# Performance work log

Measured on AMD Instinct MI355X. Metric: run time of the kernel, lower is better.

Reference implementation:

```python
import jax, jax.numpy as jnp
import numpy as np

CHEB_K = 3
HIDDEN = 64
HORIZON = 12
OUT_DIM = 1


def _supports(E, K):
    # adaptive adjacency: softmax(relu(E E^T)) rows, Chebyshev polynomial stack [K, N, N]
    A = jax.nn.softmax(jax.nn.relu(E @ E.T), axis=1)
    N = E.shape[0]
    s = [jnp.eye(N, dtype=E.dtype), A]
    for _ in range(2, K):
        s.append(2.0 * (A @ s[-1]) - s[-2])
    return jnp.stack(s, axis=0)


def _gconv(x, supports, W, b):
    # x: [B,N,C], supports: [K,N,N], W: [N,K,C,O], b: [N,O] -> [B,N,O]
    xg = jnp.einsum('knm,bmc->bnkc', supports, x)
    return jnp.einsum('bnkc,nkco->bno', xg, W) + b


def _agcrn_layer(x_seq, supports, gW, gb, uW, ub):
    # x_seq: [B,T,N,C]; returns full hidden sequence [B,T,N,H]
    B, T, N, _ = x_seq.shape
    h0 = jnp.zeros((B, N, HIDDEN), dtype=x_seq.dtype)

    def step(h, x):
        zr = jax.nn.sigmoid(_gconv(jnp.concatenate([x, h], axis=-1), supports, gW, gb))
        z, r = zr[..., :HIDDEN], zr[..., HIDDEN:]
        hc = jnp.tanh(_gconv(jnp.concatenate([x, z * h], axis=-1), supports, uW, ub))
        h_new = r * h + (1.0 - r) * hc
        return h_new, h_new

    _, hs = jax.lax.scan(step, h0, jnp.swapaxes(x_seq, 0, 1))  # [T,B,N,H]
    return jnp.swapaxes(hs, 0, 1)


def _forward(source, E, pools, conv_w, conv_b):
    supports = _supports(E, CHEB_K)
    cur = source
    for (gwp, gbp, uwp, ubp) in pools:
        # per-node weights from embedding pool (hoisted: E is constant over time)
        gW = jnp.einsum('nd,dkio->nkio', E, gwp)
        gb = E @ gbp
        uW = jnp.einsum('nd,dkio->nkio', E, uwp)
        ub = E @ ubp
        cur = _agcrn_layer(cur, supports, gW, gb, uW, ub)
    last = cur[:, -1]  # [B,N,H]
    # end_conv: Conv2d(1, horizon*out_dim, kernel=(1,H)) == linear over H per node
    y = jnp.einsum('bnh,oh->bon', last, conv_w) + conv_b[None, :, None]  # [B, horizon*out, N]
    B, _, N = y.shape
    y = y.reshape(B, HORIZON, OUT_DIM, N).transpose(0, 1, 3, 2)  # [B, horizon, N, out_dim]
    return y


def setup_inputs() -> dict:
    key = jax.random.key(0)
    ks = jax.random.split(key, 12)
    B, T, N, C, D, H = 64, 12, 2000, 1, 16, HIDDEN
    s = 0.1  # keep gates/tanh unsaturated
    return {
        'source': jax.random.normal(ks[0], (B, T, N, C), jnp.float32),
        'node_embeddings': jax.random.normal(ks[1], (N, D), jnp.float32),
        'gate_wpool_0': jax.random.normal(ks[2], (D, CHEB_K, C + H, 2 * H), jnp.float32) * s,
        'gate_bpool_0': jax.random.normal(ks[3], (D, 2 * H), jnp.float32) * s,
        'update_wpool_0': jax.random.normal(ks[4], (D, CHEB_K, C + H, H), jnp.float32) * s,
        'update_bpool_0': jax.random.normal(ks[5], (D, H), jnp.float32) * s,
        'gate_wpool_1': jax.random.normal(ks[6], (D, CHEB_K, 2 * H, 2 * H), jnp.float32) * s,
        'gate_bpool_1': jax.random.normal(ks[7], (D, 2 * H), jnp.float32) * s,
        'update_wpool_1': jax.random.normal(ks[8], (D, CHEB_K, 2 * H, H), jnp.float32) * s,
        'update_bpool_1': jax.random.normal(ks[9], (D, H), jnp.float32) * s,
        'conv_w': jax.random.normal(ks[10], (HORIZON * OUT_DIM, H), jnp.float32) * s,
        'conv_b': jax.random.normal(ks[11], (HORIZON * OUT_DIM,), jnp.float32) * s,
    }


def reference(source, node_embeddings, gate_wpool_0, gate_bpool_0, update_wpool_0,
              update_bpool_0, gate_wpool_1, gate_bpool_1, update_wpool_1,
              update_bpool_1, conv_w, conv_b):
    pools = [
        (gate_wpool_0, gate_bpool_0, update_wpool_0, update_bpool_0),
        (gate_wpool_1, gate_bpool_1, update_wpool_1, update_bpool_1),
    ]
    return _forward(source, node_embeddings, pools, conv_w, conv_b)
```

## Files before the change

### kernel.cpp

```cpp
#include <hip/hip_runtime.h>
#include <hip/hip_bf16.h>
#include <math.h>

#define NN 2000
#define DD 16
#define BB 64
#define TT 12
#define HH 64
#define MR 4000
#define SCL 2048.0f
#define ISCL (1.0f / 2048.0f)

typedef _Float16 f16;
typedef __attribute__((ext_vector_type(8))) _Float16 frag8h;
typedef __attribute__((ext_vector_type(4))) float floatx4;

__device__ inline float fin(float v) {
  return (v == v && v > -1e30f && v < 1e30f) ? v : 0.f;
}
__device__ inline float sigmoid_safe(float x) {
  float e = expf(-fabsf(x));
  float s = 1.f / (1.f + e);
  return x >= 0.f ? s : 1.f - s;
}
__device__ inline float tanh_safe(float x) {
  float e = expf(-2.f * fabsf(x));
  float r = (1.f - e) / (1.f + e);
  return x >= 0.f ? r : -r;
}
__device__ inline void split16(float v, f16& hi, f16& lo) {
  hi = (f16)v;
  lo = (f16)((v - (float)hi) * SCL);
}
__device__ inline void gll16(const void* g, void* l) {
  __builtin_amdgcn_global_load_lds((const __attribute__((address_space(1))) void*)g,
                                   (__attribute__((address_space(3))) void*)l, 16, 0, 0);
}

__global__ void kzero(float* p, int n) {
  int i = blockIdx.x * 256 + threadIdx.x;
  if (i < n) p[i] = 0.f;
}

__global__ __launch_bounds__(256) void ka(const float* __restrict__ E,
                                          float* __restrict__ A) {
  __shared__ float s[NN];
  __shared__ float red[256];
  int n = blockIdx.x;
  float en[DD];
#pragma unroll
  for (int d = 0; d < DD; ++d) en[d] = fin(E[n * DD + d]);
  float lmax = 0.f;
  for (int m = threadIdx.x; m < NN; m += 256) {
    float acc = 0.f;
#pragma unroll
    for (int d = 0; d < DD; ++d) acc += en[d] * fin(E[m * DD + d]);
    acc = fmaxf(acc, 0.f);
    s[m] = acc;
    lmax = fmaxf(lmax, acc);
  }
  red[threadIdx.x] = lmax;
  __syncthreads();
  for (int w = 128; w > 0; w >>= 1) {
    if (threadIdx.x < w) red[threadIdx.x] = fmaxf(red[threadIdx.x], red[threadIdx.x + w]);
    __syncthreads();
  }
  float mx = red[0];
  __syncthreads();
  float lsum = 0.f;
  for (int m = threadIdx.x; m < NN; m += 256) {
    float e = expf(s[m] - mx);
    s[m] = e;
    lsum += e;
  }
  red[threadIdx.x] = lsum;
  __syncthreads();
  for (int w = 128; w > 0; w >>= 1) {
    if (threadIdx.x < w) red[threadIdx.x] += red[threadIdx.x + w];
    __syncthreads();
  }
  float inv = 1.f / red[0];
  for (int m = threadIdx.x; m < NN; m += 256) A[(size_t)n * NN + m] = s[m] * inv;
}

#define TM 64
#define TK 32
__global__ __launch_bounds__(256) void kg(const float* __restrict__ A,
                                          const float* __restrict__ V,
                                          float* __restrict__ C, int cols) {
  __shared__ float As[TK][TM + 1];
  __shared__ float Bs[TK][TM + 1];
  int r0 = blockIdx.x * TM;
  int c0 = blockIdx.y * TM;
  int tid = threadIdx.x;
  int tx = tid % 16;
  int ty = tid / 16;
  float acc[4][4];
#pragma unroll
  for (int i = 0; i < 4; ++i)
#pragma unroll
    for (int j = 0; j < 4; ++j) acc[i][j] = 0.f;
  for (int k0 = 0; k0 < NN; k0 += TK) {
    for (int i = tid; i < TM * TK; i += 256) {
      int rr = i / TK, kk = i % TK;
      int gr = r0 + rr, gk = k0 + kk;
      As[kk][rr] = (gr < NN && gk < NN) ? A[(size_t)gr * NN + gk] : 0.f;
    }
    for (int i = tid; i < TK * TM; i += 256) {
      int kk = i / TM, cc = i % TM;
      int gk = k0 + kk, gc = c0 + cc;
      Bs[kk][cc] = (gk < NN && gc < cols) ? V[(size_t)gk * cols + gc] : 0.f;
    }
    __syncthreads();
#pragma unroll 4
    for (int kk = 0; kk < TK; ++kk) {
      float a[4], b[4];
#pragma unroll
      for (int i = 0; i < 4; ++i) a[i] = As[kk][ty * 4 + i];
#pragma unroll
      for (int j = 0; j < 4; ++j) b[j] = Bs[kk][tx * 4 + j];
#pragma unroll
      for (int i = 0; i < 4; ++i)
#pragma unroll
        for (int j = 0; j < 4; ++j) acc[i][j] += a[i] * b[j];
    }
    __syncthreads();
  }
#pragma unroll
  for (int i = 0; i < 4; ++i) {
    int gr = r0 + ty * 4 + i;
    if (gr >= NN) continue;
#pragma unroll
    for (int j = 0; j < 4; ++j) {
      int gc = c0 + tx * 4 + j;
      if (gc < cols) C[(size_t)gr * cols + gc] = acc[i][j];
    }
  }
}

__global__ void ksplitM(const float* __restrict__ A, const float* __restrict__ A2,
                        f16* __restrict__ Mh, f16* __restrict__ Ml) {
  int i = blockIdx.x * 256 + threadIdx.x;
  if (i >= MR * NN) return;
  int m = i / NN;
  int k = i % NN;
  float v;
  if (m < NN) v = A[(size_t)m * NN + k];
  else {
    int mm = m - NN;
    v = 2.f * A2[(size_t)mm * NN + k] - (mm == k ? 1.f : 0.f);
  }
  f16 hi, lo;
  split16(v, hi, lo);
  Mh[i] = hi;
  Ml[i] = lo;
}

__global__ __launch_bounds__(256) void kconvT(const float* __restrict__ V,
                                              f16* __restrict__ Th,
                                              f16* __restrict__ Tl, int cols) {
  __shared__ float sh[32][33];
  int k0 = blockIdx.x * 32;
  int c0 = blockIdx.y * 32;
  int tx = threadIdx.x % 32;
  int ty = threadIdx.x / 32;
#pragma unroll
  for (int i = 0; i < 4; ++i) {
    int r = k0 + ty + i * 8;
    int c = c0 + tx;
    sh[ty + i * 8][tx] = (r < NN && c < cols) ? V[(size_t)r * cols + c] : 0.f;
  }
  __syncthreads();
#pragma unroll
  for (int i = 0; i < 4; ++i) {
    int cc = c0 + ty + i * 8;
    int kk = k0 + tx;
    if (cc < cols && kk < NN) {
      f16 hi, lo;
      split16(sh[tx][ty + i * 8], hi, lo);
      Th[(size_t)cc * NN + kk] = hi;
      Tl[(size_t)cc * NN + kk] = lo;
    }
  }
}

#define KT 32
__global__ __launch_bounds__(256, 2) void kmm(const f16* __restrict__ Mh,
                                              const f16* __restrict__ Ml,
                                              const f16* __restrict__ Bh,
                                              const f16* __restrict__ Bl,
                                              float* __restrict__ C1,
                                              float* __restrict__ C2, int cols) {
  __shared__ __align__(16) f16 Ash[128 * KT];
  __shared__ __align__(16) f16 Asl[128 * KT];
  __shared__ __align__(16) f16 Bsh[128 * KT];
  __shared__ __align__(16) f16 Bsl[128 * KT];
  int tid = threadIdx.x;
  int lane = tid & 63;
  int wave = tid >> 6;
  int wr = wave >> 1;
  int wc = wave & 1;
  int bx = blockIdx.x;
  int by = blockIdx.y;
  floatx4 acc0[4][4], acc1[4][4];
#pragma unroll
  for (int i = 0; i < 4; ++i)
#pragma unroll
    for (int j = 0; j < 4; ++j) {
      acc0[i][j] = (floatx4){0.f, 0.f, 0.f, 0.f};
      acc1[i][j] = (floatx4){0.f, 0.f, 0.f, 0.f};
    }
  const frag8h zf = {0, 0, 0, 0, 0, 0, 0, 0};

  auto comp = [&]() {
    frag8h ah[4], al[4], bh[4], bl[4];
#pragma unroll
    for (int mi = 0; mi < 4; ++mi) {
      int jr = wr * 4 + mi;
      ah[mi] = *(const frag8h*)(&Ash[jr * 512 + lane * 8]);
      al[mi] = *(const frag8h*)(&Asl[jr * 512 + lane * 8]);
    }
#pragma unroll
    for (int ni = 0; ni < 4; ++ni) {
      int jc = wc * 4 + ni;
      bh[ni] = *(const frag8h*)(&Bsh[jc * 512 + lane * 8]);
      bl[ni] = *(const frag8h*)(&Bsl[jc * 512 + lane * 8]);
    }
#pragma unroll
    for (int mi = 0; mi < 4; ++mi)
#pragma unroll
      for (int ni = 0; ni < 4; ++ni) {
        acc0[mi][ni] = __builtin_amdgcn_mfma_f32_16x16x32_f16(ah[mi], bh[ni], acc0[mi][ni], 0, 0, 0);
        acc1[mi][ni] = __builtin_amdgcn_mfma_f32_16x16x32_f16(ah[mi], bl[ni], acc1[mi][ni], 0, 0, 0);
        acc1[mi][ni] = __builtin_amdgcn_mfma_f32_16x16x32_f16(al[mi], bh[ni], acc1[mi][ni], 0, 0, 0);
      }
  };

  const int lr = lane & 15;
  const int lq = lane >> 4;
  for (int k0 = 0; k0 + KT <= NN; k0 += KT) {
#pragma unroll
    for (int jj = 0; jj < 2; ++jj) {
      int j = wave * 2 + jj;
      int r = j * 16 + lr;
      size_t ko = (size_t)k0 + lq * 8;
      int gra = bx * 128 + r;
      if (gra < MR) {
        gll16(Mh + (size_t)gra * NN + ko, Ash + j * 512);
        gll16(Ml + (size_t)gra * NN + ko, Asl + j * 512);
      }
      int grb = by * 128 + r;
      if (grb < cols) {
        gll16(Bh + (size_t)grb * NN + ko, Bsh + j * 512);
        gll16(Bl + (size_t)grb * NN + ko, Bsl + j * 512);
      }
    }
    __syncthreads();
    comp();
    __syncthreads();
  }
  {
    int k0 = (NN / KT) * KT;
    if (k0 < NN) {
      for (int c = tid; c < 512; c += 256) {
        int j = c >> 6;
        int ll = c & 63;
        int q = ll >> 4;
        int rr = ll & 15;
        int r = j * 16 + rr;
        int gk = k0 + q * 8;
        bool kok = (gk + 8 <= NN);
        int gra = bx * 128 + r;
        bool aok = kok && (gra < MR);
        size_t ga = (size_t)gra * NN + gk;
        *(frag8h*)(&Ash[c * 8]) = aok ? *(const frag8h*)(Mh + ga) : zf;
        *(frag8h*)(&Asl[c * 8]) = aok ? *(const frag8h*)(Ml + ga) : zf;
        int grb = by * 128 + r;
        bool bok = kok && (grb < cols);
        size_t gb = (size_t)grb * NN + gk;
        *(frag8h*)(&Bsh[c * 8]) = bok ? *(const frag8h*)(Bh + gb) : zf;
        *(frag8h*)(&Bsl[c * 8]) = bok ? *(const frag8h*)(Bl + gb) : zf;
      }
      __syncthreads();
      comp();
      __syncthreads();
    }
  }
#pragma unroll
  for (int mi = 0; mi < 4; ++mi) {
#pragma unroll
    for (int ni = 0; ni < 4; ++ni) {
#pragma unroll
      for (int reg = 0; reg < 4; ++reg) {
        int row = bx * 128 + wr * 64 + mi * 16 + (lane >> 4) * 4 + reg;
        int col = by * 128 + wc * 64 + ni * 16 + (lane & 15);
        if (col >= cols || row >= MR) continue;
        float v = acc0[mi][ni][reg] + acc1[mi][ni][reg] * ISCL;
        if (row < NN) C1[(size_t)row * cols + col] = v;
        else C2[(size_t)(row - NN) * cols + col] = v;
      }
    }
  }
}

__global__ void kx(const float* __restrict__ src, float* __restrict__ xb,
                   int t, int b0, int CB) {
  int i = blockIdx.x * 256 + threadIdx.x;
  if (i >= NN * CB) return;
  int bb = i % CB;
  int n = i / CB;
  xb[i] = fin(src[((size_t)(b0 + bb) * TT + t) * NN + n]);
}

__global__ void kmulz(float* __restrict__ zb, const float* __restrict__ h, int n) {
  int i = blockIdx.x * 256 + threadIdx.x;
  if (i < n) zb[i] = zb[i] * h[i];
}

template <int O, int CB>
__global__ __launch_bounds__(256) void kgc(
    const float* __restrict__ x0, const float* __restrict__ x1, const float* __restrict__ x2,
    const float* __restrict__ wp, int Ctot, int base_c, int nC,
    const float* __restrict__ E, const float* __restrict__ bp,
    int act, int accum, float* outA, float* outB,
    int update, const float* __restrict__ rb, float* hio) {
  __shared__ float xs[8][CB + 1];
  __shared__ float ws[8][O];
  __shared__ float esm[DD];
  int n = blockIdx.x;
  int tid = threadIdx.x;
  int to = tid % 16;
  int tb = tid / 16;
  if (tid < DD) esm[tid] = fin(E[n * DD + tid]);
  __syncthreads();
  constexpr int NO = O / 16;
  constexpr int NB = CB / 16;
  float acc[NB][NO];
#pragma unroll
  for (int i = 0; i < NB; ++i)
#pragma unroll
    for (int j = 0; j < NO; ++j) acc[i][j] = 0.f;
  const size_t nb = (size_t)n * CB;
  for (int k = 0; k < 3; ++k) {
    const float* xk = (k == 0) ? x0 : (k == 1) ? x1 : x2;
    for (int c0 = 0; c0 < nC; c0 += 8) {
      int chunk = (nC - c0 < 8) ? (nC - c0) : 8;
      for (int i = tid; i < chunk * CB; i += 256) {
        int cc = i % chunk;
        int b = i / chunk;
        xs[cc][b] = xk[(nb + b) * nC + c0 + cc];
      }
      for (int i = tid; i < chunk * O; i += 256) {
        int o = i % O;
        int cc = i / O;
        int crow = base_c + c0 + cc;
        float wa = 0.f;
#pragma unroll
        for (int d = 0; d < DD; ++d)
          wa += esm[d] * fin(wp[((size_t)(d * 3 + k) * Ctot + crow) * O + o]);
        ws[cc][o] = wa;
      }
      __syncthreads();
      for (int cc = 0; cc < chunk; ++cc) {
        float xv[NB];
#pragma unroll
        for (int i = 0; i < NB; ++i) xv[i] = xs[cc][tb + 16 * i];
#pragma unroll
        for (int j = 0; j < NO; ++j) {
          float wv = ws[cc][to + 16 * j];
#pragma unroll
          for (int i = 0; i < NB; ++i) acc[i][j] += xv[i] * wv;
        }
      }
      __syncthreads();
    }
  }
#pragma unroll
  for (int i2 = 0; i2 < NB; ++i2) {
    int b = tb + 16 * i2;
#pragma unroll
    for (int j = 0; j < NO; ++j) {
      int o = to + 16 * j;
      float r = acc[i2][j];
      float* dst = (o < HH || !outB) ? (outA + (nb + b) * HH + (o % HH))
                                     : (outB + (nb + b) * HH + (o - HH));
      if (accum) r += *dst;
      if (bp) {
        float ba = 0.f;
#pragma unroll
        for (int d = 0; d < DD; ++d) ba += esm[d] * fin(bp[d * O + o]);
        r += ba;
      }
      r = fin(r);
      if (act == 1) r = sigmoid_safe(r);
      else if (act == 2) r = tanh_safe(r);
      if (update) {
        float rg = rb[(nb + b) * HH + o];
        float hold = hio[(nb + b) * HH + o];
        hio[(nb + b) * HH + o] = rg * hold + (1.f - rg) * r;
      } else {
        *dst = r;
      }
    }
  }
}

__global__ void kfin(const float* __restrict__ h1, const float* __restrict__ cw,
                     const float* __restrict__ cb, float* __restrict__ out,
                     int b0, int CB) {
  int idx = blockIdx.x * 256 + threadIdx.x;
  if (idx >= CB * TT * NN) return;
  int n = idx % NN;
  int o = (idx / NN) % TT;
  int bb = idx / (NN * TT);
  const float* hp = h1 + ((size_t)n * CB + bb) * HH;
  float acc = fin(cb[o]);
#pragma unroll
  for (int hh = 0; hh < HH; ++hh) acc += hp[hh] * fin(cw[o * HH + hh]);
  out[((size_t)(b0 + bb) * TT + o) * NN + n] = fin(acc);
}

template <int CB>
static void run_chunks(const float* src, const float* E,
                       const float* gwp0, const float* gbp0,
                       const float* uwp0, const float* ubp0,
                       const float* gwp1, const float* gbp1,
                       const float* uwp1, const float* ubp1,
                       const float* cw, const float* cb,
                       float* out, f16* Mh, f16* Ml,
                       char* wsp, size_t off0, hipStream_t stream) {
  size_t off = off0;
  auto allocf = [&](size_t nelem) {
    float* p = (float*)(wsp + off);
    off += (nelem * 4 + 255) & ~(size_t)255;
    return p;
  };
  auto alloch = [&](size_t nelem) {
    f16* p = (f16*)(wsp + off);
    off += (nelem * 2 + 255) & ~(size_t)255;
    return p;
  };
  const int C = CB * HH;
  const size_t NC = (size_t)NN * C;
  float* P1  = allocf(NC);
  float* P2  = allocf(NC);
  float* h0  = allocf(NC);
  float* h1  = allocf(NC);
  float* zb  = allocf(NC);
  float* rbf = allocf(NC);
  float* hc  = allocf(NC);
  f16* vh = alloch(NC);
  f16* vl = alloch(NC);
  float* xb0 = allocf((size_t)NN * CB);
  float* xb1 = allocf((size_t)NN * CB);
  float* xb2 = allocf((size_t)NN * CB);
  f16* xth = alloch((size_t)NN * CB);
  f16* xtl = alloch((size_t)NN * CB);

  const int EW = (int)((NC + 255) / 256);
  const int EWS = (NN * CB + 255) / 256;
  const dim3 gConv((NN + 31) / 32, (C + 31) / 32);
  const dim3 gConvX((NN + 31) / 32, (CB + 31) / 32);
  const dim3 gMM((MR + 127) / 128, (C + 127) / 128);
  const dim3 gMMX((MR + 127) / 128, (CB + 127) / 128);
  float* nul = nullptr;

  auto chain = [&](const float* V) {
    kconvT<<<gConv, 256, 0, stream>>>(V, vh, vl, C);
    kmm<<<gMM, 256, 0, stream>>>(Mh, Ml, vh, vl, P1, P2, C);
  };

  for (int b0 = 0; b0 < BB; b0 += CB) {
    kzero<<<EW, 256, 0, stream>>>(h0, (int)NC);
    kzero<<<EW, 256, 0, stream>>>(h1, (int)NC);
    for (int t = 0; t < TT; ++t) {
      kx<<<EWS, 256, 0, stream>>>(src, xb0, t, b0, CB);
      kconvT<<<gConvX, 256, 0, stream>>>(xb0, xth, xtl, CB);
      kmm<<<gMMX, 256, 0, stream>>>(Mh, Ml, xth, xtl, xb1, xb2, CB);
      chain(h0);
      kgc<128, CB><<<NN, 256, 0, stream>>>(h0, P1, P2, gwp0, 65, 1, 64, E, nullptr,
                                           0, 0, zb, rbf, 0, nul, nul);
      kgc<128, CB><<<NN, 256, 0, stream>>>(xb0, xb1, xb2, gwp0, 65, 0, 1, E, gbp0,
                                           1, 1, zb, rbf, 0, nul, nul);
      kgc<64, CB><<<NN, 256, 0, stream>>>(xb0, xb1, xb2, uwp0, 65, 0, 1, E, nullptr,
                                          0, 0, hc, nul, 0, nul, nul);
      kmulz<<<EW, 256, 0, stream>>>(zb, h0, (int)NC);
      chain(zb);
      kgc<64, CB><<<NN, 256, 0, stream>>>(zb, P1, P2, uwp0, 65, 1, 64, E, ubp0,
                                          2, 1, hc, nul, 1, rbf, h0);
      chain(h1);
      kgc<128, CB><<<NN, 256, 0, stream>>>(h1, P1, P2, gwp1, 128, 64, 64, E, nullptr,
                                           0, 0, zb, rbf, 0, nul, nul);
      chain(h0);
      kgc<128, CB><<<NN, 256, 0, stream>>>(h0, P1, P2, gwp1, 128, 0, 64, E, gbp1,
                                           1, 1, zb, rbf, 0, nul, nul);
      kgc<64, CB><<<NN, 256, 0, stream>>>(h0, P1, P2, uwp1, 128, 0, 64, E, nullptr,
                                          0, 0, hc, nul, 0, nul, nul);
      kmulz<<<EW, 256, 0, stream>>>(zb, h1, (int)NC);
      chain(zb);
      kgc<64, CB><<<NN, 256, 0, stream>>>(zb, P1, P2, uwp1, 128, 64, 64, E, ubp1,
                                          2, 1, hc, nul, 1, rbf, h1);
    }
    kfin<<<(CB * TT * NN + 255) / 256, 256, 0, stream>>>(h1, cw, cb, out, b0, CB);
  }
}

extern "C" void kernel_launch(void* const* d_in, const int* in_sizes, int n_in,
                              void* d_out, int out_size, void* d_ws, size_t ws_size,
                              hipStream_t stream) {
  const float* src  = (const float*)d_in[0];
  const float* E    = (const float*)d_in[1];
  const float* gwp0 = (const float*)d_in[2];
  const float* gbp0 = (const float*)d_in[3];
  const float* uwp0 = (const float*)d_in[4];
  const float* ubp0 = (const float*)d_in[5];
  const float* gwp1 = (const float*)d_in[6];
  const float* gbp1 = (const float*)d_in[7];
  const float* uwp1 = (const float*)d_in[8];
  const float* ubp1 = (const float*)d_in[9];
  const float* cw   = (const float*)d_in[10];
  const float* cb   = (const float*)d_in[11];
  float* out = (float*)d_out;
  (void)in_sizes; (void)n_in; (void)out_size;

  char* wsp = (char*)d_ws;
  size_t off = 0;
  f16* Mh = (f16*)(wsp + off); off += ((size_t)MR * NN * 2 + 255) & ~(size_t)255;
  f16* Ml = (f16*)(wsp + off); off += ((size_t)MR * NN * 2 + 255) & ~(size_t)255;
  size_t off0 = off;
  float* A  = (float*)(wsp + off0);
  float* A2 = (float*)(wsp + off0 + (((size_t)NN * NN * 4 + 255) & ~(size_t)255));

  ka<<<NN, 256, 0, stream>>>(E, A);
  {
    dim3 g((NN + TM - 1) / TM, (NN + TM - 1) / TM);
    kg<<<g, 256, 0, stream>>>(A, A, A2, NN);
  }
  ksplitM<<<(MR * NN + 255) / 256, 256, 0, stream>>>(A, A2, Mh, Ml);

  if (ws_size >= (size_t)320 * 1000 * 1000) {
    run_chunks<64>(src, E, gwp0, gbp0, uwp0, ubp0, gwp1, gbp1, uwp1, ubp1,
                   cw, cb, out, Mh, Ml, wsp, off0, stream);
  } else if (ws_size >= (size_t)185 * 1000 * 1000) {
    run_chunks<32>(src, E, gwp0, gbp0, uwp0, ubp0, gwp1, gbp1, uwp1, ubp1,
                   cw, cb, out, Mh, Ml, wsp, off0, stream);
  } else {
    run_chunks<16>(src, E, gwp0, gbp0, uwp0, ubp0, gwp1, gbp1, uwp1, ubp1,
                   cw, cb, out, Mh, Ml, wsp, off0, stream);
  }
}
```

Before: 61.84 ms.

## Swizzle block order in kmm and hoist load address computation

Remaps the linear block index so that groups of 8 consecutive blocks share column tiles, which is meant to improve L2 reuse of the M operand across the grid. Global load pointers, bounds checks and LDS offsets are precomputed outside the k loop and advanced incrementally, cutting per-iteration integer work. The inner compute loads A fragments per row instead of all at once, lowering peak register pressure. The swizzle only applies when gridDim.y is a multiple of 8 and relies on the remap being a bijection.

```diff
diff --git a/kernel.cpp b/kernel.cpp
--- a/kernel.cpp
+++ b/kernel.cpp
@@ -202,6 +202,16 @@
   int wc = wave & 1;
   int bx = blockIdx.x;
   int by = blockIdx.y;
+  {
+    int cy = gridDim.y, rx = gridDim.x;
+    if (cy % 8 == 0 && cy > 1) {
+      int per = cy / 8;
+      int lin = by * rx + bx;
+      int m = lin >> 3;
+      by = (lin & 7) * per + (m % per);
+      bx = m / per;
+    }
+  }
   floatx4 acc0[4][4], acc1[4][4];
 #pragma unroll
   for (int i = 0; i < 4; ++i)
@@ -212,52 +222,64 @@
     }
   const frag8h zf = {0, 0, 0, 0, 0, 0, 0, 0};
 
-  auto comp = [&]() {
-    frag8h ah[4], al[4], bh[4], bl[4];
-#pragma unroll
-    for (int mi = 0; mi < 4; ++mi) {
-      int jr = wr * 4 + mi;
-      ah[mi] = *(const frag8h*)(&Ash[jr * 512 + lane * 8]);
-      al[mi] = *(const frag8h*)(&Asl[jr * 512 + lane * 8]);
-    }
-#pragma unroll
-    for (int ni = 0; ni < 4; ++ni) {
-      int jc = wc * 4 + ni;
-      bh[ni] = *(const frag8h*)(&Bsh[jc * 512 + lane * 8]);
-      bl[ni] = *(const frag8h*)(&Bsl[jc * 512 + lane * 8]);
-    }
-#pragma unroll
-    for (int mi = 0; mi < 4; ++mi)
-#pragma unroll
-      for (int ni = 0; ni < 4; ++ni) {
-        acc0[mi][ni] = __builtin_amdgcn_mfma_f32_16x16x32_f16(ah[mi], bh[ni], acc0[mi][ni], 0, 0, 0);
-        acc1[mi][ni] = __builtin_amdgcn_mfma_f32_16x16x32_f16(ah[mi], bl[ni], acc1[mi][ni], 0, 0, 0);
-        acc1[mi][ni] = __builtin_amdgcn_mfma_f32_16x16x32_f16(al[mi], bh[ni], acc1[mi][ni], 0, 0, 0);
-      }
-  };
-
   const int lr = lane & 15;
   const int lq = lane >> 4;
+  const int j0 = wave * 2, j1 = wave * 2 + 1;
+  const int ra0 = bx * 128 + j0 * 16 + lr;
+  const int ra1 = bx * 128 + j1 * 16 + lr;
+  const int rb0 = by * 128 + j0 * 16 + lr;
+  const int rb1 = by * 128 + j1 * 16 + lr;
+  const bool okA0 = ra0 < MR, okA1 = ra1 < MR;
+  const bool okB0 = rb0 < cols, okB1 = rb1 < cols;
+  const f16* pA0h = Mh + (size_t)ra0 * NN + lq * 8;
+  const f16* pA0l = Ml + (size_t)ra0 * NN + lq * 8;
+  const f16* pA1h = Mh + (size_t)ra1 * NN + lq * 8;
+  const f16* pA1l = Ml + (size_t)ra1 * NN + lq * 8;
+  const f16* pB0h = Bh + (size_t)rb0 * NN + lq * 8;
+  const f16* pB0l = Bl + (size_t)rb0 * NN + lq * 8;
+  const f16* pB1h = Bh + (size_t)rb1 * NN + lq * 8;
+  const f16* pB1l = Bl + (size_t)rb1 * NN + lq * 8;
+  f16* dA0h = Ash + j0 * 512; f16* dA0l = Asl + j0 * 512;
+  f16* dA1h = Ash + j1 * 512; f16* dA1l = Asl + j1 * 512;
+  f16* dB0h = Bsh + j0 * 512; f16* dB0l = Bsl + j0 * 512;
+  f16* dB1h = Bsh + j1 * 512; f16* dB1l = Bsl + j1 * 512;
+  int lofsA[4], lofsB[4];
+#pragma unroll
+  for (int i = 0; i < 4; ++i) {
+    lofsA[i] = (wr * 4 + i) * 512 + lane * 8;
+    lofsB[i] = (wc * 4 + i) * 512 + lane * 8;
+  }
+
+  auto comp = [&]() {
+    frag8h bhv[4], blv[4];
+#pragma unroll
+    for (int ni = 0; ni < 4; ++ni) {
+      bhv[ni] = *(const frag8h*)(&Bsh[lofsB[ni]]);
+      blv[ni] = *(const frag8h*)(&Bsl[lofsB[ni]]);
+    }
+#pragma unroll
+    for (int mi = 0; mi < 4; ++mi) {
+      frag8h ah = *(const frag8h*)(&Ash[lofsA[mi]]);
+      frag8h al = *(const frag8h*)(&Asl[lofsA[mi]]);
+#pragma unroll
+      for (int ni = 0; ni < 4; ++ni) {
+        acc0[mi][ni] = __builtin_amdgcn_mfma_f32_16x16x32_f16(ah, bhv[ni], acc0[mi][ni], 0, 0, 0);
+        acc1[mi][ni] = __builtin_amdgcn_mfma_f32_16x16x32_f16(ah, blv[ni], acc1[mi][ni], 0, 0, 0);
+        acc1[mi][ni] = __builtin_amdgcn_mfma_f32_16x16x32_f16(al, bhv[ni], acc1[mi][ni], 0, 0, 0);
+      }
+    }
+  };
+
   for (int k0 = 0; k0 + KT <= NN; k0 += KT) {
-#pragma unroll
-    for (int jj = 0; jj < 2; ++jj) {
-      int j = wave * 2 + jj;
-      int r = j * 16 + lr;
-      size_t ko = (size_t)k0 + lq * 8;
-      int gra = bx * 128 + r;
-      if (gra < MR) {
-        gll16(Mh + (size_t)gra * NN + ko, Ash + j * 512);
-        gll16(Ml + (size_t)gra * NN + ko, Asl + j * 512);
-      }
-      int grb = by * 128 + r;
-      if (grb < cols) {
-        gll16(Bh + (size_t)grb * NN + ko, Bsh + j * 512);
-        gll16(Bl + (size_t)grb * NN + ko, Bsl + j * 512);
-      }
-    }
+    if (okA0) { gll16(pA0h, dA0h); gll16(pA0l, dA0l); }
+    if (okA1) { gll16(pA1h, dA1h); gll16(pA1l, dA1l); }
+    if (okB0) { gll16(pB0h, dB0h); gll16(pB0l, dB0l); }
+    if (okB1) { gll16(pB1h, dB1h); gll16(pB1l, dB1l); }
     __syncthreads();
     comp();
     __syncthreads();
+    pA0h += KT; pA0l += KT; pA1h += KT; pA1l += KT;
+    pB0h += KT; pB0l += KT; pB1h += KT; pB1l += KT;
   }
   {
     int k0 = (NN / KT) * KT;
```

Result: no change. 62.93 ms (+1.8%).
